# Performance work log

Measured on AMD Instinct MI355X. Metric: run time of the kernel, lower is better.

## Reference

```python
import jax, jax.numpy as jnp
import numpy as np

B, T, D, K = 8, 2048, 384, 64

def setup_inputs() -> dict:
    key = jax.random.key(0)
    k1, k2, k3, k4 = jax.random.split(key, 4)
    x = jax.random.normal(k1, (B, T, D), dtype=jnp.float32)
    # torch nn.Linear default init scale ~ 1/sqrt(fan_in); use scaled normals
    Wq = jax.random.normal(k2, (D, K), dtype=jnp.float32) / np.sqrt(D)
    Wk = jax.random.normal(k3, (D, K), dtype=jnp.float32) / np.sqrt(D)
    Wv = jax.random.normal(k4, (D, D), dtype=jnp.float32) / np.sqrt(D)
    return {"x": x, "Wq": Wq, "Wk": Wk, "Wv": Wv}

def reference(x, Wq, Wk, Wv):
    # x: (B,T,D)
    q = jnp.einsum('btd,dk->btk', x, Wq)      # (B,T,K)
    k = jnp.einsum('btd,dk->btk', x, Wk)      # (B,T,K)
    v = jnp.einsum('btd,de->bte', x, Wv)      # (B,T,D)
    scores = jnp.einsum('bqk,bsk->bqs', q, k) / jnp.sqrt(jnp.float32(K))  # (B,T,T)
    causal = jnp.tril(jnp.ones((T, T), dtype=bool))
    scores = jnp.where(causal, scores, -jnp.inf)
    weights = jax.nn.softmax(scores, axis=-1)
    out = jnp.einsum('bqs,bse->bqe', weights, v)  # (B,T,D)
    return out
```

## Files before the change

kernel.cpp:

```cpp
#include <hip/hip_runtime.h>

#define TT 2048
#define DD 384

typedef float f32x4 __attribute__((ext_vector_type(4)));
typedef float f32x16 __attribute__((ext_vector_type(16)));
typedef short s16x8 __attribute__((ext_vector_type(8)));
typedef short s16x2 __attribute__((ext_vector_type(2)));
typedef unsigned int u32x4 __attribute__((ext_vector_type(4)));
typedef unsigned int u32x2 __attribute__((ext_vector_type(2)));

typedef __attribute__((address_space(3))) unsigned char* as3p;
typedef const __attribute__((address_space(1))) unsigned char* as1p;
#define GLLDS(gsrc, ldst) __builtin_amdgcn_global_load_lds((as1p)(gsrc), (as3p)(ldst), 16, 0, 0)

static __device__ __forceinline__ unsigned short f2bf(float f) {
    unsigned int u = __builtin_bit_cast(unsigned int, f);
    u = (u + 0x7fffu + ((u >> 16) & 1u)) >> 16;
    return (unsigned short)u;
}
static __device__ __forceinline__ unsigned int pk2(float a, float b) {
#if __has_builtin(__builtin_amdgcn_cvt_pk_bf16_f32)
    s16x2 t = __builtin_amdgcn_cvt_pk_bf16_f32(a, b);
    return __builtin_bit_cast(unsigned int, t);
#else
    unsigned int ua = __builtin_bit_cast(unsigned int, a);
    unsigned int ub = __builtin_bit_cast(unsigned int, b);
    ua = (ua + 0x7fffu + ((ua >> 16) & 1u)) >> 16;
    ub = (ub + 0x7fffu + ((ub >> 16) & 1u)) & 0xffff0000u;
    return ua | ub;
#endif
}

__global__ __launch_bounds__(256, 8) void wprep(
    const float* __restrict__ Wq, const float* __restrict__ Wk, const float* __restrict__ Wv,
    unsigned short* __restrict__ wall)
{
    const int gid = blockIdx.x * 256 + threadIdx.x;
    const int col = gid & 511;
    const int kt  = gid >> 9;
    unsigned short* op = wall + (size_t)col * 384 + kt * 32;
    #pragma unroll
    for (int c = 0; c < 4; ++c) {
        u32x4 v;
        #pragma unroll
        for (int j2 = 0; j2 < 4; ++j2) {
            const int k = kt * 32 + c * 8 + j2 * 2;
            float f0 = (col < 64)  ? Wq[(size_t)k * 64 + col]
                     : (col < 128) ? Wk[(size_t)k * 64 + (col - 64)]
                                   : Wv[(size_t)k * 384 + (col - 128)];
            float f1 = (col < 64)  ? Wq[(size_t)(k + 1) * 64 + col]
                     : (col < 128) ? Wk[(size_t)(k + 1) * 64 + (col - 64)]
                                   : Wv[(size_t)(k + 1) * 384 + (col - 128)];
            v[j2] = pk2(f0, f1);
        }
        *(s16x8*)(op + ((c ^ (col & 3)) * 8)) = __builtin_bit_cast(s16x8, v);
    }
}

__global__ __launch_bounds__(256, 4) void qkv_gemm(
    const float* __restrict__ x, const unsigned short* __restrict__ wall,
    unsigned short* __restrict__ qo, unsigned short* __restrict__ ko,
    unsigned short* __restrict__ vto)
{
    __shared__ __align__(16) unsigned short lds[12288];
    const int tid = threadIdx.x;
    const int l   = tid & 63;
    const int w   = tid >> 6;
    const int si  = l & 15;
    const int qq  = l >> 4;
    const int m0  = blockIdx.x * 64;
    const int nb  = blockIdx.y;
    const int wr  = w >> 1, wc = w & 1;

    const int ar = tid >> 2, ac = tid & 3;
    const float* xs = x + (size_t)(m0 + ar) * DD + ac * 8;
    const unsigned short* ws = wall + (size_t)nb * 128 * 384;

#define QSTAGE(KT, B)                                                                      \
    {                                                                                      \
        _Pragma("unroll")                                                                  \
        for (int c2 = 0; c2 < 2; ++c2) {                                                   \
            const int ch = w * 2 + c2;                                                     \
            GLLDS(ws + (size_t)(ch * 16 + (l >> 2)) * 384 + (KT) * 32 + (l & 3) * 8,       \
                  &lds[(B) * 6144 + 2048 + ch * 512]);                                     \
        }                                                                                  \
        f32x4 x0 = *(const f32x4*)(xs + (KT) * 32);                                        \
        f32x4 x1 = *(const f32x4*)(xs + (KT) * 32 + 4);                                    \
        u32x4 av = (u32x4){pk2(x0[0], x0[1]), pk2(x0[2], x0[3]),                           \
                           pk2(x1[0], x1[1]), pk2(x1[2], x1[3])};                          \
        *(s16x8*)&lds[(B) * 6144 + ar * 32 + ((ac ^ (ar & 3)) * 8)] =                      \
            __builtin_bit_cast(s16x8, av);                                                 \
    }

    f32x4 acc[2][4];
    #pragma unroll
    for (int rt = 0; rt < 2; ++rt)
        #pragma unroll
        for (int ct = 0; ct < 4; ++ct) acc[rt][ct] = (f32x4){0.f, 0.f, 0.f, 0.f};

    QSTAGE(0, 0);
    for (int kt = 0; kt < 12; ++kt) {
        const int b = kt & 1;
        __syncthreads();
        if (kt < 11) QSTAGE(kt + 1, 1 - b);

        s16x8 af[2], bf[4];
        #pragma unroll
        for (int rt = 0; rt < 2; ++rt) {
            const int row = wr * 32 + rt * 16 + si;
            af[rt] = *(const s16x8*)&lds[b * 6144 + row * 32 + ((qq ^ (row & 3)) * 8)];
        }
        #pragma unroll
        for (int ct = 0; ct < 4; ++ct) {
            const int col = wc * 64 + ct * 16 + si;
            bf[ct] = *(const s16x8*)&lds[b * 6144 + 2048 + col * 32 + ((qq ^ (col & 3)) * 8)];
        }
        #pragma unroll
        for (int rt = 0; rt < 2; ++rt)
            #pragma unroll
            for (int ct = 0; ct < 4; ++ct)
                acc[rt][ct] = __builtin_amdgcn_mfma_f32_16x16x32_bf16(af[rt], bf[ct], acc[rt][ct], 0, 0, 0);
    }
    __syncthreads();
#undef QSTAGE

    if (nb == 0) {
        if (wc == 0) {
            #pragma unroll
            for (int rt = 0; rt < 2; ++rt)
                #pragma unroll
                for (int ct = 0; ct < 4; ++ct)
                    #pragma unroll
                    for (int r = 0; r < 4; ++r) {
                        const int m = m0 + wr * 32 + rt * 16 + qq * 4 + r;
                        qo[(size_t)m * 64 + ct * 16 + si] = f2bf(acc[rt][ct][r] * 0.125f);
                    }
        } else {
            #pragma unroll
            for (int rt = 0; rt < 2; ++rt)
                #pragma unroll
                for (int ct = 0; ct < 4; ++ct)
                    #pragma unroll
                    for (int r = 0; r < 4; ++r) {
                        const int m = m0 + wr * 32 + rt * 16 + qq * 4 + r;
                        const int col = ct * 16 + si;
                        ko[(size_t)m * 64 + (((col >> 3) ^ (m & 7)) * 8) + (col & 7)] = f2bf(acc[rt][ct][r]);
                    }
        }
    } else {
        #pragma unroll
        for (int rt = 0; rt < 2; ++rt)
            #pragma unroll
            for (int ct = 0; ct < 4; ++ct)
                #pragma unroll
                for (int r = 0; r < 4; ++r) {
                    const int m = wr * 32 + rt * 16 + qq * 4 + r;
                    const int n = wc * 64 + ct * 16 + si;
                    lds[n * 64 + (((m >> 3) ^ (n & 7)) * 8) + (m & 7)] = f2bf(acc[rt][ct][r]);
                }
        __syncthreads();
        const int bbat = m0 >> 11, t0 = m0 & 2047;
        #pragma unroll
        for (int i = 0; i < 4; ++i) {
            const int u = tid + 256 * i, n = u >> 3, p = u & 7;
            *(s16x8*)&vto[((size_t)bbat * DD + ((nb - 1) * 128 + n)) * TT + t0 + p * 8]
                = *(const s16x8*)&lds[n * 64 + p * 8];
        }
    }
}

__global__ __launch_bounds__(1024, 4) void attn(
    const unsigned short* __restrict__ qg, const unsigned short* __restrict__ kg,
    const unsigned short* __restrict__ vg, float* __restrict__ out)
{
    __shared__ __align__(16) unsigned short lds[53248];

    const int tid = threadIdx.x;
    const int l   = tid & 63;
    const int w   = tid >> 6;
    const bool isprod = (w < 4);
    const int qh  = isprod ? (w & 1) : ((w - 4) & 1);
    const int su  = isprod ? (w >> 1) : ((w - 4) >> 1);
    const int lo  = l & 31;
    const int hi  = l >> 5;

    const int g  = blockIdx.x;
    const int bb = g & 7;
    const int eh = (g >> 3) & 1;
    const int pr = g >> 4;
    const int e0 = eh * 192;

    const unsigned short* kbase = kg + (size_t)bb * TT * 64;
    const unsigned short* vbase = vg + ((size_t)bb * DD + e0) * TT;

    #define STAGE(IT, KB, VB)                                                              \
    {                                                                                      \
        if (isprod) {                                                                      \
            GLLDS(kbase + (size_t)(IT) * 4096 + (2 * w) * 512 + l * 8,                     \
                  &lds[(KB) * 4096 + (2 * w) * 512]);                                      \
            GLLDS(kbase + (size_t)(IT) * 4096 + (2 * w + 1) * 512 + l * 8,                 \
                  &lds[(KB) * 4096 + (2 * w + 1) * 512]);                                  \
        } else {                                                                           \
            _Pragma("unroll")                                                              \
            for (int c2 = 0; c2 < 2; ++c2) {                                               \
                const int rg = 2 * (w - 4) + c2;                                           \
                GLLDS(vbase + (size_t)(rg * 8 + (l >> 3)) * TT + (IT) * 64 + (l & 7) * 8,  \
                      &lds[8192 + (VB) * 12288 + rg * 512]);                               \
            }                                                                              \
        }                                                                                  \
    }

    #define PVSTEP(VB, PB)                                                                 \
    {                                                                                      \
        __builtin_amdgcn_s_setprio(1);                                                     \
        _Pragma("unroll")                                                                  \
        for (int ss = 0; ss < 2; ++ss) {                                                   \
            const int pbse = 45056 + (PB) * 4096 + (qh * 2 + ss) * 1024;                   \
            s16x8 a0 = *(const s16x8*)&lds[pbse + l * 8];                                  \
            s16x8 a1 = *(const s16x8*)&lds[pbse + 512 + l * 8];                            \
            const int el = su * 32 + lo;                                                   \
            const int vbse = 8192 + (VB) * 12288 + el * 64;                                \
            s16x8 v0 = *(const s16x8*)&lds[vbse + (((ss * 4 + hi) ^ (el & 7)) * 8)];       \
            o = __builtin_amdgcn_mfma_f32_32x32x16_bf16(a0, v0, o, 0, 0, 0);               \
            s16x8 v1 = *(const s16x8*)&lds[vbse + (((ss * 4 + 2 + hi) ^ (el & 7)) * 8)];   \
            o = __builtin_amdgcn_mfma_f32_32x32x16_bf16(a1, v1, o, 0, 0, 0);               \
        }                                                                                  \
        __builtin_amdgcn_s_setprio(0);                                                     \
    }

    for (int hf = 0; hf < 2; ++hf) {
        const int q2 = hf ? pr : 31 - pr;
        const int q0 = q2 * 64;
        const int qrow = q0 + qh * 32 + lo;

        s16x8 qf[4];
        if (isprod) {
            const unsigned short* qp = qg + ((size_t)bb * TT + qrow) * 64;
            #pragma unroll
            for (int st = 0; st < 4; ++st) qf[st] = *(const s16x8*)(qp + st * 16 + hi * 8);
        }

        f32x16 o;
        #pragma unroll
        for (int r = 0; r < 16; ++r) o[r] = 0.f;
        float lp = 0.f;

        STAGE(0, 0, 0);

        int vi = 0, vn = 1;
        for (int it = 0; it <= q2; ++it) {
            const int kb = it & 1;
            __syncthreads();

            if (it < q2) STAGE(it + 1, 1 - kb, vn);

            if (isprod) {
                f32x16 sa;
                #pragma unroll
                for (int r = 0; r < 16; ++r) sa[r] = 0.f;
                __builtin_amdgcn_s_setprio(1);
                #pragma unroll
                for (int st = 0; st < 4; ++st) {
                    s16x8 kf = *(const s16x8*)&lds[kb * 4096 + (su * 32 + lo) * 64 + (((st * 2 + hi) ^ (lo & 7)) * 8)];
                    sa = __builtin_amdgcn_mfma_f32_32x32x16_bf16(kf, qf[st], sa, 0, 0, 0);
                }
                __builtin_amdgcn_s_setprio(0);
                const bool mb = (it == q2);
                float pv[16];
                #pragma unroll
                for (int r = 0; r < 16; ++r) {
                    float e = __expf(sa[r]);
                    if (mb) {
                        const int srow = it * 64 + su * 32 + (r & 3) + 8 * (r >> 2) + 4 * hi;
                        if (srow > qrow) e = 0.f;
                    }
                    pv[r] = e;
                    lp += e;
                }
                unsigned int d0 = pk2(pv[0], pv[1]),   d1 = pk2(pv[2], pv[3]);
                unsigned int d2 = pk2(pv[4], pv[5]),   d3 = pk2(pv[6], pv[7]);
                unsigned int d4 = pk2(pv[8], pv[9]),   d5 = pk2(pv[10], pv[11]);
                unsigned int d6 = pk2(pv[12], pv[13]), d7 = pk2(pv[14], pv[15]);
                u32x4 fa0, fa1;
#if __has_builtin(__builtin_amdgcn_permlane32_swap)
                {
                    u32x2 s02 = __builtin_bit_cast(u32x2, __builtin_amdgcn_permlane32_swap(d0, d2, false, false));
                    u32x2 s13 = __builtin_bit_cast(u32x2, __builtin_amdgcn_permlane32_swap(d1, d3, false, false));
                    u32x2 s46 = __builtin_bit_cast(u32x2, __builtin_amdgcn_permlane32_swap(d4, d6, false, false));
                    u32x2 s57 = __builtin_bit_cast(u32x2, __builtin_amdgcn_permlane32_swap(d5, d7, false, false));
                    fa0 = (u32x4){s02[0], s13[0], s02[1], s13[1]};
                    fa1 = (u32x4){s46[0], s57[0], s46[1], s57[1]};
                }
#else
                {
                    unsigned int sA0 = hi ? d0 : d2, sA1 = hi ? d1 : d3;
                    unsigned int rA0 = (unsigned int)__shfl_xor((int)sA0, 32);
                    unsigned int rA1 = (unsigned int)__shfl_xor((int)sA1, 32);
                    fa0 = hi ? (u32x4){rA0, rA1, d2, d3} : (u32x4){d0, d1, rA0, rA1};
                    unsigned int sB0 = hi ? d4 : d6, sB1 = hi ? d5 : d7;
                    unsigned int rB0 = (unsigned int)__shfl_xor((int)sB0, 32);
                    unsigned int rB1 = (unsigned int)__shfl_xor((int)sB1, 32);
                    fa1 = hi ? (u32x4){rB0, rB1, d6, d7} : (u32x4){d4, d5, rB0, rB1};
                }
#endif
                *(s16x8*)&lds[45056 + kb * 4096 + (qh * 2 + su) * 1024 + l * 8]       = __builtin_bit_cast(s16x8, fa0);
                *(s16x8*)&lds[45056 + kb * 4096 + (qh * 2 + su) * 1024 + 512 + l * 8] = __builtin_bit_cast(s16x8, fa1);
            } else if (it > 0) {
                const int vp = (vi == 0) ? 2 : vi - 1;
                PVSTEP(vp, 1 - kb);
            }

            vi = vn; vn = (vn == 2) ? 0 : vn + 1;
        }
        __syncthreads();

        if (isprod) {
            float lt = lp + __shfl_xor(lp, 32);
            if (hi == 0) ((float*)lds)[(qh * 2 + su) * 32 + lo] = lt;
        } else {
            const int vlast = (vi == 0) ? 2 : vi - 1;
            PVSTEP(vlast, q2 & 1);
        }
        __syncthreads();

        if (!isprod) {
            const float* stL = (const float*)lds;
            #pragma unroll
            for (int r = 0; r < 16; ++r) {
                const int rloc = (r & 3) + 8 * (r >> 2) + 4 * hi;
                const float linv = 1.f / (stL[(qh * 2) * 32 + rloc] + stL[(qh * 2 + 1) * 32 + rloc]);
                out[((size_t)bb * TT + q0 + qh * 32 + rloc) * DD + e0 + su * 32 + lo]
                    = o[r] * linv;
            }
        }
        __syncthreads();
    }
    #undef STAGE
    #undef PVSTEP
}

extern "C" void kernel_launch(void* const* d_in, const int* in_sizes, int n_in,
                              void* d_out, int out_size, void* d_ws, size_t ws_size,
                              hipStream_t stream)
{
    const float* x  = (const float*)d_in[0];
    const float* Wq = (const float*)d_in[1];
    const float* Wk = (const float*)d_in[2];
    const float* Wv = (const float*)d_in[3];

    unsigned short* qws  = (unsigned short*)d_ws;
    unsigned short* kws  = (unsigned short*)((char*)d_ws + ((size_t)2 << 20));
    unsigned short* vtws = (unsigned short*)((char*)d_ws + ((size_t)4 << 20));
    unsigned short* wall = (unsigned short*)((char*)d_ws + ((size_t)16 << 20));

    wprep<<<dim3(24), dim3(256), 0, stream>>>(Wq, Wk, Wv, wall);
    qkv_gemm<<<dim3(256, 4), dim3(256), 0, stream>>>(x, wall, qws, kws, vtws);
    attn<<<dim3(256), dim3(1024), 0, stream>>>(qws, kws, vtws, (float*)d_out);
}
```

Baseline: 126.0 us.

## Split attention into one query tile per block with 512-thread blocks

The attention kernel now runs 512 blocks of 512 threads instead of 256 blocks of 1024. Each block handles a single 64-row query tile, where before each block processed a paired long and short tile one after the other. The four consumer waves now each compute three 32-wide output column tiles (96 columns) rather than one, and they issue six V staging loads apiece. The aim is finer-grained scheduling across CUs and fewer threads per block, at the cost of more accumulator registers per consumer wave and less balanced work per block.

```diff
diff --git a/kernel.cpp b/kernel.cpp
--- a/kernel.cpp
+++ b/kernel.cpp
@@ -170,7 +170,7 @@
     }
 }
 
-__global__ __launch_bounds__(1024, 4) void attn(
+__global__ __launch_bounds__(512, 4) void attn(
     const unsigned short* __restrict__ qg, const unsigned short* __restrict__ kg,
     const unsigned short* __restrict__ vg, float* __restrict__ out)
 {
@@ -188,7 +188,9 @@
     const int g  = blockIdx.x;
     const int bb = g & 7;
     const int eh = (g >> 3) & 1;
-    const int pr = g >> 4;
+    const int s  = g >> 4;
+    const int q2 = (s < 16) ? (31 - s) : (s - 16);
+    const int q0 = q2 * 64;
     const int e0 = eh * 192;
 
     const unsigned short* kbase = kg + (size_t)bb * TT * 64;
@@ -203,8 +205,8 @@
                   &lds[(KB) * 4096 + (2 * w + 1) * 512]);                                  \
         } else {                                                                           \
             _Pragma("unroll")                                                              \
-            for (int c2 = 0; c2 < 2; ++c2) {                                               \
-                const int rg = 2 * (w - 4) + c2;                                           \
+            for (int c6 = 0; c6 < 6; ++c6) {                                               \
+                const int rg = 6 * (w - 4) + c6;                                           \
                 GLLDS(vbase + (size_t)(rg * 8 + (l >> 3)) * TT + (IT) * 64 + (l & 7) * 8,  \
                       &lds[8192 + (VB) * 12288 + rg * 512]);                               \
             }                                                                              \
@@ -219,122 +221,124 @@
             const int pbse = 45056 + (PB) * 4096 + (qh * 2 + ss) * 1024;                   \
             s16x8 a0 = *(const s16x8*)&lds[pbse + l * 8];                                  \
             s16x8 a1 = *(const s16x8*)&lds[pbse + 512 + l * 8];                            \
-            const int el = su * 32 + lo;                                                   \
-            const int vbse = 8192 + (VB) * 12288 + el * 64;                                \
-            s16x8 v0 = *(const s16x8*)&lds[vbse + (((ss * 4 + hi) ^ (el & 7)) * 8)];       \
-            o = __builtin_amdgcn_mfma_f32_32x32x16_bf16(a0, v0, o, 0, 0, 0);               \
-            s16x8 v1 = *(const s16x8*)&lds[vbse + (((ss * 4 + 2 + hi) ^ (el & 7)) * 8)];   \
-            o = __builtin_amdgcn_mfma_f32_32x32x16_bf16(a1, v1, o, 0, 0, 0);               \
+            _Pragma("unroll")                                                              \
+            for (int et = 0; et < 3; ++et) {                                               \
+                const int el = su * 96 + et * 32 + lo;                                     \
+                const int vbse = 8192 + (VB) * 12288 + el * 64;                            \
+                s16x8 v0 = *(const s16x8*)&lds[vbse + (((ss * 4 + hi) ^ (el & 7)) * 8)];   \
+                o[et] = __builtin_amdgcn_mfma_f32_32x32x16_bf16(a0, v0, o[et], 0, 0, 0);   \
+                s16x8 v1 = *(const s16x8*)&lds[vbse + (((ss * 4 + 2 + hi) ^ (el & 7)) * 8)]; \
+                o[et] = __builtin_amdgcn_mfma_f32_32x32x16_bf16(a1, v1, o[et], 0, 0, 0);   \
+            }                                                                              \
         }                                                                                  \
         __builtin_amdgcn_s_setprio(0);                                                     \
     }
 
-    for (int hf = 0; hf < 2; ++hf) {
-        const int q2 = hf ? pr : 31 - pr;
-        const int q0 = q2 * 64;
-        const int qrow = q0 + qh * 32 + lo;
-
-        s16x8 qf[4];
+    const int qrow = q0 + qh * 32 + lo;
+
+    s16x8 qf[4];
+    if (isprod) {
+        const unsigned short* qp = qg + ((size_t)bb * TT + qrow) * 64;
+        #pragma unroll
+        for (int st = 0; st < 4; ++st) qf[st] = *(const s16x8*)(qp + st * 16 + hi * 8);
+    }
+
+    f32x16 o[3];
+    #pragma unroll
+    for (int et = 0; et < 3; ++et)
+        #pragma unroll
+        for (int r = 0; r < 16; ++r) o[et][r] = 0.f;
+    float lp = 0.f;
+
+    STAGE(0, 0, 0);
+
+    int vi = 0, vn = 1;
+    for (int it = 0; it <= q2; ++it) {
+        const int kb = it & 1;
+        __syncthreads();
+
+        if (it < q2) STAGE(it + 1, 1 - kb, vn);
+
         if (isprod) {
-            const unsigned short* qp = qg + ((size_t)bb * TT + qrow) * 64;
-            #pragma unroll
-            for (int st = 0; st < 4; ++st) qf[st] = *(const s16x8*)(qp + st * 16 + hi * 8);
-        }
-
-        f32x16 o;
-        #pragma unroll
-        for (int r = 0; r < 16; ++r) o[r] = 0.f;
-        float lp = 0.f;
-
-        STAGE(0, 0, 0);
-
-        int vi = 0, vn = 1;
-        for (int it = 0; it <= q2; ++it) {
-            const int kb = it & 1;
-            __syncthreads();
-
-            if (it < q2) STAGE(it + 1, 1 - kb, vn);
-
-            if (isprod) {
-                f32x16 sa;
-                #pragma unroll
-                for (int r = 0; r < 16; ++r) sa[r] = 0.f;
-                __builtin_amdgcn_s_setprio(1);
-                #pragma unroll
-                for (int st = 0; st < 4; ++st) {
-                    s16x8 kf = *(const s16x8*)&lds[kb * 4096 + (su * 32 + lo) * 64 + (((st * 2 + hi) ^ (lo & 7)) * 8)];
-                    sa = __builtin_amdgcn_mfma_f32_32x32x16_bf16(kf, qf[st], sa, 0, 0, 0);
+            f32x16 sa;
+            #pragma unroll
+            for (int r = 0; r < 16; ++r) sa[r] = 0.f;
+            __builtin_amdgcn_s_setprio(1);
+            #pragma unroll
+            for (int st = 0; st < 4; ++st) {
+                s16x8 kf = *(const s16x8*)&lds[kb * 4096 + (su * 32 + lo) * 64 + (((st * 2 + hi) ^ (lo & 7)) * 8)];
+                sa = __builtin_amdgcn_mfma_f32_32x32x16_bf16(kf, qf[st], sa, 0, 0, 0);
+            }
+            __builtin_amdgcn_s_setprio(0);
+            const bool mb = (it == q2);
+            float pv[16];
+            #pragma unroll
+            for (int r = 0; r < 16; ++r) {
+                float e = __expf(sa[r]);
+                if (mb) {
+                    const int srow = it * 64 + su * 32 + (r & 3) + 8 * (r >> 2) + 4 * hi;
+                    if (srow > qrow) e = 0.f;
                 }
-                __builtin_amdgcn_s_setprio(0);
-                const bool mb = (it == q2);
-                float pv[16];
-                #pragma unroll
-                for (int r = 0; r < 16; ++r) {
-                    float e = __expf(sa[r]);
-                    if (mb) {
-                        const int srow = it * 64 + su * 32 + (r & 3) + 8 * (r >> 2) + 4 * hi;
-                        if (srow > qrow) e = 0.f;
-                    }
-                    pv[r] = e;
-                    lp += e;
-                }
-                unsigned int d0 = pk2(pv[0], pv[1]),   d1 = pk2(pv[2], pv[3]);
-                unsigned int d2 = pk2(pv[4], pv[5]),   d3 = pk2(pv[6], pv[7]);
-                unsigned int d4 = pk2(pv[8], pv[9]),   d5 = pk2(pv[10], pv[11]);
-                unsigned int d6 = pk2(pv[12], pv[13]), d7 = pk2(pv[14], pv[15]);
-                u32x4 fa0, fa1;
+                pv[r] = e;
+                lp += e;
+            }
+            unsigned int d0 = pk2(pv[0], pv[1]),   d1 = pk2(pv[2], pv[3]);
+            unsigned int d2 = pk2(pv[4], pv[5]),   d3 = pk2(pv[6], pv[7]);
+            unsigned int d4 = pk2(pv[8], pv[9]),   d5 = pk2(pv[10], pv[11]);
+            unsigned int d6 = pk2(pv[12], pv[13]), d7 = pk2(pv[14], pv[15]);
+            u32x4 fa0, fa1;
 #if __has_builtin(__builtin_amdgcn_permlane32_swap)
-                {
-                    u32x2 s02 = __builtin_bit_cast(u32x2, __builtin_amdgcn_permlane32_swap(d0, d2, false, false));
-                    u32x2 s13 = __builtin_bit_cast(u32x2, __builtin_amdgcn_permlane32_swap(d1, d3, false, false));
-                    u32x2 s46 = __builtin_bit_cast(u32x2, __builtin_amdgcn_permlane32_swap(d4, d6, false, false));
-                    u32x2 s57 = __builtin_bit_cast(u32x2, __builtin_amdgcn_permlane32_swap(d5, d7, false, false));
-                    fa0 = (u32x4){s02[0], s13[0], s02[1], s13[1]};
-                    fa1 = (u32x4){s46[0], s57[0], s46[1], s57[1]};
-                }
+            {
+                u32x2 s02 = __builtin_bit_cast(u32x2, __builtin_amdgcn_permlane32_swap(d0, d2, false, false));
+                u32x2 s13 = __builtin_bit_cast(u32x2, __builtin_amdgcn_permlane32_swap(d1, d3, false, false));
+                u32x2 s46 = __builtin_bit_cast(u32x2, __builtin_amdgcn_permlane32_swap(d4, d6, false, false));
+                u32x2 s57 = __builtin_bit_cast(u32x2, __builtin_amdgcn_permlane32_swap(d5, d7, false, false));
+                fa0 = (u32x4){s02[0], s13[0], s02[1], s13[1]};
+                fa1 = (u32x4){s46[0], s57[0], s46[1], s57[1]};
+            }
 #else
-                {
-                    unsigned int sA0 = hi ? d0 : d2, sA1 = hi ? d1 : d3;
-                    unsigned int rA0 = (unsigned int)__shfl_xor((int)sA0, 32);
-                    unsigned int rA1 = (unsigned int)__shfl_xor((int)sA1, 32);
-                    fa0 = hi ? (u32x4){rA0, rA1, d2, d3} : (u32x4){d0, d1, rA0, rA1};
-                    unsigned int sB0 = hi ? d4 : d6, sB1 = hi ? d5 : d7;
-                    unsigned int rB0 = (unsigned int)__shfl_xor((int)sB0, 32);
-                    unsigned int rB1 = (unsigned int)__shfl_xor((int)sB1, 32);
-                    fa1 = hi ? (u32x4){rB0, rB1, d6, d7} : (u32x4){d4, d5, rB0, rB1};
-                }
+            {
+                unsigned int sA0 = hi ? d0 : d2, sA1 = hi ? d1 : d3;
+                unsigned int rA0 = (unsigned int)__shfl_xor((int)sA0, 32);
+                unsigned int rA1 = (unsigned int)__shfl_xor((int)sA1, 32);
+                fa0 = hi ? (u32x4){rA0, rA1, d2, d3} : (u32x4){d0, d1, rA0, rA1};
+                unsigned int sB0 = hi ? d4 : d6, sB1 = hi ? d5 : d7;
+                unsigned int rB0 = (unsigned int)__shfl_xor((int)sB0, 32);
+                unsigned int rB1 = (unsigned int)__shfl_xor((int)sB1, 32);
+                fa1 = hi ? (u32x4){rB0, rB1, d6, d7} : (u32x4){d4, d5, rB0, rB1};
+            }
 #endif
-                *(s16x8*)&lds[45056 + kb * 4096 + (qh * 2 + su) * 1024 + l * 8]       = __builtin_bit_cast(s16x8, fa0);
-                *(s16x8*)&lds[45056 + kb * 4096 + (qh * 2 + su) * 1024 + 512 + l * 8] = __builtin_bit_cast(s16x8, fa1);
-            } else if (it > 0) {
-                const int vp = (vi == 0) ? 2 : vi - 1;
-                PVSTEP(vp, 1 - kb);
-            }
-
-            vi = vn; vn = (vn == 2) ? 0 : vn + 1;
-        }
-        __syncthreads();
-
-        if (isprod) {
-            float lt = lp + __shfl_xor(lp, 32);
-            if (hi == 0) ((float*)lds)[(qh * 2 + su) * 32 + lo] = lt;
-        } else {
-            const int vlast = (vi == 0) ? 2 : vi - 1;
-            PVSTEP(vlast, q2 & 1);
-        }
-        __syncthreads();
-
-        if (!isprod) {
-            const float* stL = (const float*)lds;
+            *(s16x8*)&lds[45056 + kb * 4096 + (qh * 2 + su) * 1024 + l * 8]       = __builtin_bit_cast(s16x8, fa0);
+            *(s16x8*)&lds[45056 + kb * 4096 + (qh * 2 + su) * 1024 + 512 + l * 8] = __builtin_bit_cast(s16x8, fa1);
+        } else if (it > 0) {
+            const int vp = (vi == 0) ? 2 : vi - 1;
+            PVSTEP(vp, 1 - kb);
+        }
+
+        vi = vn; vn = (vn == 2) ? 0 : vn + 1;
+    }
+    __syncthreads();
+
+    if (isprod) {
+        float lt = lp + __shfl_xor(lp, 32);
+        if (hi == 0) ((float*)lds)[(qh * 2 + su) * 32 + lo] = lt;
+    } else {
+        const int vlast = (vi == 0) ? 2 : vi - 1;
+        PVSTEP(vlast, q2 & 1);
+    }
+    __syncthreads();
+
+    if (!isprod) {
+        const float* stL = (const float*)lds;
+        #pragma unroll
+        for (int et = 0; et < 3; ++et)
             #pragma unroll
             for (int r = 0; r < 16; ++r) {
                 const int rloc = (r & 3) + 8 * (r >> 2) + 4 * hi;
                 const float linv = 1.f / (stL[(qh * 2) * 32 + rloc] + stL[(qh * 2 + 1) * 32 + rloc]);
-                out[((size_t)bb * TT + q0 + qh * 32 + rloc) * DD + e0 + su * 32 + lo]
-                    = o[r] * linv;
-            }
-        }
-        __syncthreads();
+                out[((size_t)bb * TT + q0 + qh * 32 + rloc) * DD + e0 + su * 96 + et * 32 + lo]
+                    = o[et][r] * linv;
+            }
     }
     #undef STAGE
     #undef PVSTEP
@@ -356,5 +360,5 @@
 
     wprep<<<dim3(24), dim3(256), 0, stream>>>(Wq, Wk, Wv, wall);
     qkv_gemm<<<dim3(256, 4), dim3(256), 0, stream>>>(x, wall, qws, kws, vtws);
-    attn<<<dim3(256), dim3(1024), 0, stream>>>(qws, kws, vtws, (float*)d_out);
-}
+    attn<<<dim3(512), dim3(512), 0, stream>>>(qws, kws, vtws, (float*)d_out);
+}
```

After: 134.1 us. +6.5%, slower.
